# Optimization experiments

Hardware: AMD Instinct MI355X
Metric: run time of the kernel (lower is better)

The kernel has to match this reference:

```python
import jax, jax.numpy as jnp
import numpy as np

SOS = 0
MAX_LENGTH = 64

N_LATENTS = 256
N_CHARACTERS = 128
N_HIDDENS = 1024
BATCH = 4096


def setup_inputs() -> dict:
    key = jax.random.key(0)
    ks = jax.random.split(key, 16)
    H, L, C = N_HIDDENS, N_LATENTS, N_CHARACTERS
    s = 0.02
    return {
        "z": jax.random.normal(ks[0], (BATCH, L), dtype=jnp.float32),
        "embed_w": jax.random.normal(ks[1], (C, H), dtype=jnp.float32) * s,
        "z2h_w": jax.random.normal(ks[2], (H, L), dtype=jnp.float32) * s,
        "z2h_b": jnp.zeros((H,), dtype=jnp.float32),
        "w_ih0": jax.random.normal(ks[3], (3 * H, H + L), dtype=jnp.float32) * s,
        "w_hh0": jax.random.normal(ks[4], (3 * H, H), dtype=jnp.float32) * s,
        "b_ih0": jnp.zeros((3 * H,), dtype=jnp.float32),
        "b_hh0": jnp.zeros((3 * H,), dtype=jnp.float32),
        "w_ih1": jax.random.normal(ks[5], (3 * H, H), dtype=jnp.float32) * s,
        "w_hh1": jax.random.normal(ks[6], (3 * H, H), dtype=jnp.float32) * s,
        "b_ih1": jnp.zeros((3 * H,), dtype=jnp.float32),
        "b_hh1": jnp.zeros((3 * H,), dtype=jnp.float32),
        "h2o_w": jax.random.normal(ks[7], (C, H + L), dtype=jnp.float32) * s,
        "h2o_b": jnp.zeros((C,), dtype=jnp.float32),
    }


def _gru_cell(x, h, w_ih, w_hh, b_ih, b_hh):
    # PyTorch GRUCell math. x: [B, I], h: [B, H]
    gi = x @ w_ih.T + b_ih  # [B, 3H]
    gh = h @ w_hh.T + b_hh  # [B, 3H]
    i_r, i_z, i_n = jnp.split(gi, 3, axis=1)
    h_r, h_z, h_n = jnp.split(gh, 3, axis=1)
    r = jax.nn.sigmoid(i_r + h_r)
    zg = jax.nn.sigmoid(i_z + h_z)
    n = jnp.tanh(i_n + r * h_n)
    return (1.0 - zg) * n + zg * h


def reference(z, embed_w, z2h_w, z2h_b,
              w_ih0, w_hh0, b_ih0, b_hh0,
              w_ih1, w_hh1, b_ih1, b_hh1,
              h2o_w, h2o_b):
    batch = z.shape[0]
    h0 = z @ z2h_w.T + z2h_b  # [B, H], replicated across both GRU layers

    def step(carry, _):
        c_in, h1, h2 = carry
        e = embed_w[c_in]                      # [B, H] embedding lookup
        e = e * jax.nn.sigmoid(e)              # swish
        x = jnp.concatenate([e, z], axis=1)    # [B, H+L]
        h1 = _gru_cell(x, h1, w_ih0, w_hh0, b_ih0, b_hh0)
        h2 = _gru_cell(h1, h2, w_ih1, w_hh1, b_ih1, b_hh1)
        out = jnp.concatenate([h2, z], axis=1) @ h2o_w.T + h2o_b  # [B, C]
        # argmax(log_softmax(out)) == argmax(out)
        sample = jnp.argmax(out, axis=1).astype(jnp.int32)
        return (sample, h1, h2), out

    c0 = jnp.full((batch,), SOS, dtype=jnp.int32)
    _, outs = jax.lax.scan(step, (c0, h0, h0), None, length=MAX_LENGTH)
    return jnp.transpose(outs, (1, 0, 2))  # [B, T, C]
```

## Files before the change

### kernel.cpp

```cpp
#include <hip/hip_runtime.h>
#include <hip/hip_bf16.h>
#include <stdint.h>
#include <stddef.h>

#define B_   4096
#define H_   1024
#define L_   256
#define C_   128
#define T_   64
#define H3_  3072

typedef unsigned short u16;
typedef __attribute__((ext_vector_type(8))) short bf16x8;
typedef __attribute__((ext_vector_type(4))) float f32x4;

typedef const void __attribute__((address_space(1)))* as1_cvp;
typedef void __attribute__((address_space(3)))* as3_vp;

__device__ __forceinline__ void gl2lds16(const void* g, void* l) {
  __builtin_amdgcn_global_load_lds((as1_cvp)g, (as3_vp)l, 16, 0, 0);
}

__device__ __forceinline__ float bf2f(u16 u) {
  union { float f; unsigned int i; } x; x.i = ((unsigned int)u) << 16; return x.f;
}
__device__ __forceinline__ u16 f2bf(float f) {
  union { float f; unsigned int i; } x; x.f = f;
  unsigned int r = x.i + 0x7fffu + ((x.i >> 16) & 1u);
  return (u16)(r >> 16);
}
__device__ __forceinline__ float sigm(float x) { return 1.f / (1.f + __expf(-x)); }
__device__ __forceinline__ float tanh_fast(float x) {
  float e = __expf(2.f * x); return 1.f - 2.f / (e + 1.f);
}

template<int OUT_MODE>
__device__ __forceinline__ void gemm_tile_body(
    u16* As, u16* Ws,
    const u16* __restrict__ A, int lda,
    const u16* __restrict__ W, int ldw,
    const float* __restrict__ bias,
    void* __restrict__ C0p, void* __restrict__ C1p, int ldc, int K,
    int m0, int n0)
{
  const int tid  = threadIdx.x;
  const int wave = tid >> 6, lane = tid & 63;
  const int wm = (wave >> 1) * 64, wn = (wave & 1) * 64;
  const int lrow = lane & 15, lq = lane >> 4;
  const int arow = wave * 8 + (lane >> 3);
  const int acol = (lane & 7) * 8;

  f32x4 acc[4][4] = {};

  const u16* Ag = A + (size_t)m0 * lda;
  const u16* Wg = W + (size_t)n0 * ldw;

  for (int k0 = 0; k0 < K; k0 += 64) {
    __syncthreads();
    #pragma unroll
    for (int rd = 0; rd < 4; rd++) {
      gl2lds16(Ag + (size_t)(rd * 32 + arow) * lda + (k0 + acol), As + rd * 2048 + wave * 512);
      gl2lds16(Wg + (size_t)(rd * 32 + arow) * ldw + (k0 + acol), Ws + rd * 2048 + wave * 512);
    }
    __syncthreads();
    #pragma unroll
    for (int kk = 0; kk < 64; kk += 32) {
      bf16x8 af[4], bw[4];
      #pragma unroll
      for (int i = 0; i < 4; i++)
        af[i] = *(const bf16x8*)&As[(wm + i * 16 + lrow) * 64 + kk + lq * 8];
      #pragma unroll
      for (int j = 0; j < 4; j++)
        bw[j] = *(const bf16x8*)&Ws[(wn + j * 16 + lrow) * 64 + kk + lq * 8];
      #pragma unroll
      for (int i = 0; i < 4; i++)
        #pragma unroll
        for (int j = 0; j < 4; j++)
          acc[i][j] = __builtin_amdgcn_mfma_f32_16x16x32_bf16(af[i], bw[j], acc[i][j], 0, 0, 0);
    }
  }

  #pragma unroll
  for (int j = 0; j < 4; j++) {
    const int col = n0 + wn + j * 16 + lrow;
    const float bv = bias ? bias[col] : 0.f;
    #pragma unroll
    for (int i = 0; i < 4; i++) {
      #pragma unroll
      for (int r = 0; r < 4; r++) {
        const int row = m0 + wm + i * 16 + lq * 4 + r;
        float v = acc[i][j][r] + bv;
        if (OUT_MODE == 0) {
          ((float*)C0p)[(size_t)row * ldc + col] = v;
        } else if (OUT_MODE == 1) {
          ((u16*)C0p)[(size_t)row * ldc + col] = f2bf(v);
        } else {
          u16 hv = f2bf(v);
          ((u16*)C0p)[(size_t)row * ldc + col] = hv;
          ((u16*)C1p)[(size_t)row * ldc + col] = hv;
        }
      }
    }
  }
}

template<int OUT_MODE>
__global__ __launch_bounds__(256) void gemm_bt(
    const u16* __restrict__ A, int lda,
    const u16* __restrict__ W, int ldw,
    const float* __restrict__ bias,
    void* __restrict__ C0p, void* __restrict__ C1p, int ldc, int K)
{
  __shared__ __align__(16) u16 As[128 * 64];
  __shared__ __align__(16) u16 Ws[128 * 64];
  gemm_tile_body<OUT_MODE>(As, Ws, A, lda, W, ldw, bias, C0p, C1p, ldc, K,
                           blockIdx.y * 128, blockIdx.x * 128);
}

__device__ __forceinline__ void out_body(
    u16* As, u16* Ws, int ob,
    const u16* __restrict__ h2, const u16* __restrict__ Wo,
    const float* __restrict__ Oz, float* __restrict__ outp,
    int* __restrict__ cnew, int t)
{
  const int tid = threadIdx.x, wave = tid >> 6, lane = tid & 63;
  const int b0 = ob * 64;
  const int lrow = lane & 15, lq = lane >> 4;
  const int arow = wave * 8 + (lane >> 3);
  const int acol = (lane & 7) * 8;
  f32x4 acc[8] = {};

  for (int k0 = 0; k0 < H_; k0 += 64) {
    __syncthreads();
    #pragma unroll
    for (int rd = 0; rd < 2; rd++)
      gl2lds16(h2 + (size_t)(b0 + rd * 32 + arow) * H_ + k0 + acol, As + rd * 2048 + wave * 512);
    #pragma unroll
    for (int rd = 0; rd < 4; rd++)
      gl2lds16(Wo + (size_t)(rd * 32 + arow) * H_ + k0 + acol, Ws + rd * 2048 + wave * 512);
    __syncthreads();
    #pragma unroll
    for (int kk = 0; kk < 64; kk += 32) {
      bf16x8 af = *(const bf16x8*)&As[(wave * 16 + lrow) * 64 + kk + lq * 8];
      #pragma unroll
      for (int j = 0; j < 8; j++) {
        bf16x8 bw = *(const bf16x8*)&Ws[(j * 16 + lrow) * 64 + kk + lq * 8];
        acc[j] = __builtin_amdgcn_mfma_f32_16x16x32_bf16(af, bw, acc[j], 0, 0, 0);
      }
    }
  }

  #pragma unroll
  for (int r = 0; r < 4; r++) {
    const int row = b0 + wave * 16 + lq * 4 + r;
    float mv = -3.4e38f; int mi = 0;
    #pragma unroll
    for (int j = 0; j < 8; j++) {
      const int col = j * 16 + lrow;
      float v = acc[j][r] + Oz[(size_t)row * C_ + col];
      outp[(size_t)row * (T_ * C_) + t * C_ + col] = v;
      if (v > mv) { mv = v; mi = col; }
    }
    #pragma unroll
    for (int off = 1; off < 16; off <<= 1) {
      float ov = __shfl_xor(mv, off);
      int   oi = __shfl_xor(mi, off);
      if (ov > mv || (ov == mv && oi < mi)) { mv = ov; mi = oi; }
    }
    if (lrow == 0) cnew[row] = mi;
  }
}

__global__ __launch_bounds__(256) void step1(
    const u16* __restrict__ h1, const u16* __restrict__ whh0,
    const float* __restrict__ b_hh0, u16* __restrict__ gh0,
    const u16* __restrict__ h2cur, const u16* __restrict__ Wo,
    const float* __restrict__ Oz, float* __restrict__ outp,
    int* __restrict__ cbuf, int tprev)
{
  __shared__ __align__(16) u16 As[128 * 64];
  __shared__ __align__(16) u16 Ws[128 * 64];
  int bid = blockIdx.x;
  if (bid < 64) {
    if (tprev >= 0) out_body(As, Ws, bid, h2cur, Wo, Oz, outp, cbuf, tprev);
    return;
  }
  const int g = bid - 64;
  const int xcd = g & 7, k = g >> 3;
  const int n = xcd * 3 + (k % 3);
  const int m = k / 3;
  gemm_tile_body<1>(As, Ws, h1, H_, whh0, H_, b_hh0, gh0, nullptr, H3_, H_,
                    m * 128, n * 128);
}

template<bool PH2>
__device__ __forceinline__ void l3_phase(
    u16* As, u16* Ws,
    const u16* __restrict__ Ag, const u16* __restrict__ Wg, int j0,
    f32x4 acc[3][2][4], f32x4 accN[2][4])
{
  const int tid = threadIdx.x, wave = tid >> 6, lane = tid & 63;
  const int wmh = wave >> 1, wj = wave & 1;
  const int lrow = lane & 15, lq = lane >> 4;
  const int arow = wave * 8 + (lane >> 3);
  const int acol = (lane & 7) * 8;

  for (int k0 = 0; k0 < H_; k0 += 64) {
    __syncthreads();
    #pragma unroll
    for (int rd = 0; rd < 4; rd++)
      gl2lds16(Ag + (size_t)(rd * 32 + arow) * H_ + (k0 + acol), As + rd * 2048 + wave * 512);
    #pragma unroll
    for (int rd = 0; rd < 6; rd++)
      gl2lds16(Wg + (size_t)((rd >> 1) * 1024 + j0 + (rd & 1) * 32 + arow) * H_ + (k0 + acol),
               Ws + rd * 2048 + wave * 512);
    __syncthreads();
    #pragma unroll
    for (int kk = 0; kk < 64; kk += 32) {
      bf16x8 af[4];
      #pragma unroll
      for (int i = 0; i < 4; i++)
        af[i] = *(const bf16x8*)&As[(wmh * 64 + i * 16 + lrow) * 64 + kk + lq * 8];
      #pragma unroll
      for (int g = 0; g < 3; g++) {
        #pragma unroll
        for (int u = 0; u < 2; u++) {
          bf16x8 bw = *(const bf16x8*)&Ws[(g * 64 + wj * 32 + u * 16 + lrow) * 64 + kk + lq * 8];
          #pragma unroll
          for (int i = 0; i < 4; i++) {
            if (PH2 && g == 2)
              accN[u][i] = __builtin_amdgcn_mfma_f32_16x16x32_bf16(af[i], bw, accN[u][i], 0, 0, 0);
            else
              acc[g][u][i] = __builtin_amdgcn_mfma_f32_16x16x32_bf16(af[i], bw, acc[g][u][i], 0, 0, 0);
          }
        }
      }
    }
  }
}

__global__ __launch_bounds__(256, 2) void gemm_l3(
    const u16* __restrict__ h1, const u16* __restrict__ h2old,
    const u16* __restrict__ wih1, const u16* __restrict__ whh1,
    const float* __restrict__ b_ih1, const float* __restrict__ b_hh1,
    u16* __restrict__ h2new)
{
  __shared__ __align__(16) u16 As[128 * 64];
  __shared__ __align__(16) u16 Ws[192 * 64];
  const int bid = blockIdx.x;
  const int xcd = bid & 7, k = bid >> 3;
  const int jt = xcd * 2 + (k & 1);
  const int m  = k >> 1;
  const int m0 = m * 128, j0 = jt * 64;

  f32x4 acc[3][2][4] = {};
  f32x4 accN[2][4] = {};

  l3_phase<false>(As, Ws, h1    + (size_t)m0 * H_, wih1, j0, acc, accN);
  l3_phase<true >(As, Ws, h2old + (size_t)m0 * H_, whh1, j0, acc, accN);

  const int tid = threadIdx.x, wave = tid >> 6, lane = tid & 63;
  const int wmh = wave >> 1, wj = wave & 1;
  const int lrow = lane & 15, lq = lane >> 4;

  #pragma unroll
  for (int u = 0; u < 2; u++) {
    const int j = j0 + wj * 32 + u * 16 + lrow;
    const float bR  = b_ih1[j] + b_hh1[j];
    const float bZ  = b_ih1[H_ + j] + b_hh1[H_ + j];
    const float bNi = b_ih1[2 * H_ + j];
    const float bNh = b_hh1[2 * H_ + j];
    #pragma unroll
    for (int i = 0; i < 4; i++) {
      #pragma unroll
      for (int rr = 0; rr < 4; rr++) {
        const int row = m0 + wmh * 64 + i * 16 + lq * 4 + rr;
        float r  = sigm(acc[0][u][i][rr] + bR);
        float zg = sigm(acc[1][u][i][rr] + bZ);
        float nn = tanh_fast(acc[2][u][i][rr] + bNi + r * (accN[u][i][rr] + bNh));
        float hold = bf2f(h2old[(size_t)row * H_ + j]);
        h2new[(size_t)row * H_ + j] = f2bf((1.f - zg) * nn + zg * hold);
      }
    }
  }
}

__global__ __launch_bounds__(256) void gru_cell0_v(
    const int* __restrict__ c, const u16* __restrict__ Egi,
    const u16* __restrict__ Gz, const u16* __restrict__ gh,
    u16* __restrict__ h1)
{
  const int b = blockIdx.x, j = threadIdx.x * 4;
  const u16* eg = Egi + (size_t)c[b] * H3_ + j;
  const size_t g = (size_t)b * H3_ + j;
  ushort4 er = *(const ushort4*)&eg[0];
  ushort4 ez = *(const ushort4*)&eg[H_];
  ushort4 en = *(const ushort4*)&eg[2 * H_];
  ushort4 zr = *(const ushort4*)&Gz[g];
  ushort4 zz = *(const ushort4*)&Gz[g + H_];
  ushort4 zn = *(const ushort4*)&Gz[g + 2 * H_];
  ushort4 hr = *(const ushort4*)&gh[g];
  ushort4 hz = *(const ushort4*)&gh[g + H_];
  ushort4 hn = *(const ushort4*)&gh[g + 2 * H_];
  const size_t hi = (size_t)b * H_ + j;
  ushort4 hold = *(const ushort4*)&h1[hi];
  ushort4 outv;
  #pragma unroll
  for (int k = 0; k < 4; k++) {
    float gir = bf2f(((const u16*)&er)[k]) + bf2f(((const u16*)&zr)[k]);
    float giz = bf2f(((const u16*)&ez)[k]) + bf2f(((const u16*)&zz)[k]);
    float gin = bf2f(((const u16*)&en)[k]) + bf2f(((const u16*)&zn)[k]);
    float r  = sigm(gir + bf2f(((const u16*)&hr)[k]));
    float zg = sigm(giz + bf2f(((const u16*)&hz)[k]));
    float nn = tanh_fast(gin + r * bf2f(((const u16*)&hn)[k]));
    float h = bf2f(((const u16*)&hold)[k]);
    ((u16*)&outv)[k] = f2bf((1.f - zg) * nn + zg * h);
  }
  *(ushort4*)&h1[hi] = outv;
}

__global__ __launch_bounds__(256) void conv_bf16_k(const float* __restrict__ s, u16* __restrict__ d, int n) {
  int i = blockIdx.x * 256 + threadIdx.x;
  if (i < n) d[i] = f2bf(s[i]);
}
__global__ __launch_bounds__(256) void conv_split_k(const float* __restrict__ s, u16* __restrict__ dA,
                                                    u16* __restrict__ dZ, int rows) {
  int i = blockIdx.x * 256 + threadIdx.x;
  if (i >= rows * 1280) return;
  int rr = i / 1280, col = i - rr * 1280;
  float v = s[i];
  if (col < 1024) dA[(size_t)rr * 1024 + col] = f2bf(v);
  else            dZ[(size_t)rr * 256 + (col - 1024)] = f2bf(v);
}
__global__ __launch_bounds__(256) void conv_swish_k(const float* __restrict__ s, u16* __restrict__ d, int n) {
  int i = blockIdx.x * 256 + threadIdx.x;
  if (i < n) { float e = s[i]; d[i] = f2bf(e * sigm(e)); }
}

static inline char* wsal(char*& p, size_t bytes) {
  char* r = p; p += (bytes + 255) & ~(size_t)255; return r;
}

extern "C" void kernel_launch(void* const* d_in, const int* in_sizes, int n_in,
                              void* d_out, int out_size, void* d_ws, size_t ws_size,
                              hipStream_t stream) {
  const float* z       = (const float*)d_in[0];
  const float* embed_w = (const float*)d_in[1];
  const float* z2h_w   = (const float*)d_in[2];
  const float* z2h_b   = (const float*)d_in[3];
  const float* w_ih0   = (const float*)d_in[4];
  const float* w_hh0   = (const float*)d_in[5];
  const float* b_ih0   = (const float*)d_in[6];
  const float* b_hh0   = (const float*)d_in[7];
  const float* w_ih1   = (const float*)d_in[8];
  const float* w_hh1   = (const float*)d_in[9];
  const float* b_ih1   = (const float*)d_in[10];
  const float* b_hh1   = (const float*)d_in[11];
  const float* h2o_w   = (const float*)d_in[12];
  const float* h2o_b   = (const float*)d_in[13];
  float* outp = (float*)d_out;

  char* p = (char*)d_ws;
  u16* whh0  = (u16*)wsal(p, (size_t)H3_ * H_ * 2);
  u16* wih1  = (u16*)wsal(p, (size_t)H3_ * H_ * 2);
  u16* whh1  = (u16*)wsal(p, (size_t)H3_ * H_ * 2);
  u16* wih0a = (u16*)wsal(p, (size_t)H3_ * H_ * 2);
  u16* wih0z = (u16*)wsal(p, (size_t)H3_ * L_ * 2);
  u16* h2oa  = (u16*)wsal(p, (size_t)C_ * H_ * 2);
  u16* h2oz  = (u16*)wsal(p, (size_t)C_ * L_ * 2);
  u16* z2hb  = (u16*)wsal(p, (size_t)H_ * L_ * 2);
  u16* zb    = (u16*)wsal(p, (size_t)B_ * L_ * 2);
  u16* swe   = (u16*)wsal(p, (size_t)C_ * H_ * 2);
  u16* EgiB  = (u16*)wsal(p, (size_t)C_ * H3_ * 2);
  u16* Gz    = (u16*)wsal(p, (size_t)B_ * H3_ * 2);
  float* Oz  = (float*)wsal(p, (size_t)B_ * C_ * 4);
  u16* h1    = (u16*)wsal(p, (size_t)B_ * H_ * 2);
  u16* h2a   = (u16*)wsal(p, (size_t)B_ * H_ * 2);
  u16* h2b   = (u16*)wsal(p, (size_t)B_ * H_ * 2);
  u16* gh0   = (u16*)wsal(p, (size_t)B_ * H3_ * 2);
  int* cbuf  = (int*)wsal(p, (size_t)B_ * 4);

  conv_bf16_k<<<(B_*L_ + 255)/256, 256, 0, stream>>>(z, zb, B_*L_);
  conv_bf16_k<<<(H_*L_ + 255)/256, 256, 0, stream>>>(z2h_w, z2hb, H_*L_);
  conv_bf16_k<<<(H3_*H_ + 255)/256, 256, 0, stream>>>(w_hh0, whh0, H3_*H_);
  conv_bf16_k<<<(H3_*H_ + 255)/256, 256, 0, stream>>>(w_ih1, wih1, H3_*H_);
  conv_bf16_k<<<(H3_*H_ + 255)/256, 256, 0, stream>>>(w_hh1, whh1, H3_*H_);
  conv_split_k<<<(H3_*1280 + 255)/256, 256, 0, stream>>>(w_ih0, wih0a, wih0z, H3_);
  conv_split_k<<<(C_*1280 + 255)/256, 256, 0, stream>>>(h2o_w, h2oa, h2oz, C_);
  conv_swish_k<<<(C_*H_ + 255)/256, 256, 0, stream>>>(embed_w, swe, C_*H_);
  hipMemsetAsync(cbuf, 0, B_ * sizeof(int), stream);

  gemm_bt<2><<<dim3(H_/128, B_/128), 256, 0, stream>>>(zb, L_, z2hb, L_, z2h_b, h1, h2a, H_, L_);
  gemm_bt<1><<<dim3(H3_/128, 1), 256, 0, stream>>>(swe, H_, wih0a, H_, b_ih0, EgiB, nullptr, H3_, H_);
  gemm_bt<1><<<dim3(H3_/128, B_/128), 256, 0, stream>>>(zb, L_, wih0z, L_, nullptr, Gz, nullptr, H3_, L_);
  gemm_bt<0><<<dim3(1, B_/128), 256, 0, stream>>>(zb, L_, h2oz, L_, h2o_b, Oz, nullptr, C_, L_);

  for (int t = 0; t < T_; t++) {
    const u16* h2cur = (t & 1) ? h2b : h2a;
    u16*       h2nxt = (t & 1) ? h2a : h2b;
    step1<<<832, 256, 0, stream>>>(h1, whh0, b_hh0, gh0, h2cur, h2oa, Oz, outp, cbuf, t - 1);
    gru_cell0_v<<<B_, 256, 0, stream>>>(cbuf, EgiB, Gz, gh0, h1);
    gemm_l3<<<512, 256, 0, stream>>>(h1, h2cur, wih1, whh1, b_ih1, b_hh1, h2nxt);
  }
  step1<<<64, 256, 0, stream>>>(h1, whh0, b_hh0, gh0, h2a, h2oa, Oz, outp, cbuf, T_ - 1);
}
```

Measured before the change: 8.406 ms.

## Fuse layer-0 hidden GEMM with GRU gate epilogue and split output projection

The layer-0 hidden GEMM now uses the GRU gate tiling and applies the full gate math in its epilogue. That removes the separate elementwise GRU kernel and the write and re-read of the 3H-wide gh0 buffer on every step. h1 is now double-buffered, so the new state does not overwrite the old state the epilogue still reads. The output projection and argmax move into a standalone 64-block kernel after layer 1, so it no longer overlaps with the hidden GEMM. The fused epilogue also makes narrow per-element gathers from Egi and Gz.

```diff
diff --git a/kernel.cpp b/kernel.cpp
--- a/kernel.cpp
+++ b/kernel.cpp
@@ -117,82 +117,6 @@
                            blockIdx.y * 128, blockIdx.x * 128);
 }
 
-__device__ __forceinline__ void out_body(
-    u16* As, u16* Ws, int ob,
-    const u16* __restrict__ h2, const u16* __restrict__ Wo,
-    const float* __restrict__ Oz, float* __restrict__ outp,
-    int* __restrict__ cnew, int t)
-{
-  const int tid = threadIdx.x, wave = tid >> 6, lane = tid & 63;
-  const int b0 = ob * 64;
-  const int lrow = lane & 15, lq = lane >> 4;
-  const int arow = wave * 8 + (lane >> 3);
-  const int acol = (lane & 7) * 8;
-  f32x4 acc[8] = {};
-
-  for (int k0 = 0; k0 < H_; k0 += 64) {
-    __syncthreads();
-    #pragma unroll
-    for (int rd = 0; rd < 2; rd++)
-      gl2lds16(h2 + (size_t)(b0 + rd * 32 + arow) * H_ + k0 + acol, As + rd * 2048 + wave * 512);
-    #pragma unroll
-    for (int rd = 0; rd < 4; rd++)
-      gl2lds16(Wo + (size_t)(rd * 32 + arow) * H_ + k0 + acol, Ws + rd * 2048 + wave * 512);
-    __syncthreads();
-    #pragma unroll
-    for (int kk = 0; kk < 64; kk += 32) {
-      bf16x8 af = *(const bf16x8*)&As[(wave * 16 + lrow) * 64 + kk + lq * 8];
-      #pragma unroll
-      for (int j = 0; j < 8; j++) {
-        bf16x8 bw = *(const bf16x8*)&Ws[(j * 16 + lrow) * 64 + kk + lq * 8];
-        acc[j] = __builtin_amdgcn_mfma_f32_16x16x32_bf16(af, bw, acc[j], 0, 0, 0);
-      }
-    }
-  }
-
-  #pragma unroll
-  for (int r = 0; r < 4; r++) {
-    const int row = b0 + wave * 16 + lq * 4 + r;
-    float mv = -3.4e38f; int mi = 0;
-    #pragma unroll
-    for (int j = 0; j < 8; j++) {
-      const int col = j * 16 + lrow;
-      float v = acc[j][r] + Oz[(size_t)row * C_ + col];
-      outp[(size_t)row * (T_ * C_) + t * C_ + col] = v;
-      if (v > mv) { mv = v; mi = col; }
-    }
-    #pragma unroll
-    for (int off = 1; off < 16; off <<= 1) {
-      float ov = __shfl_xor(mv, off);
-      int   oi = __shfl_xor(mi, off);
-      if (ov > mv || (ov == mv && oi < mi)) { mv = ov; mi = oi; }
-    }
-    if (lrow == 0) cnew[row] = mi;
-  }
-}
-
-__global__ __launch_bounds__(256) void step1(
-    const u16* __restrict__ h1, const u16* __restrict__ whh0,
-    const float* __restrict__ b_hh0, u16* __restrict__ gh0,
-    const u16* __restrict__ h2cur, const u16* __restrict__ Wo,
-    const float* __restrict__ Oz, float* __restrict__ outp,
-    int* __restrict__ cbuf, int tprev)
-{
-  __shared__ __align__(16) u16 As[128 * 64];
-  __shared__ __align__(16) u16 Ws[128 * 64];
-  int bid = blockIdx.x;
-  if (bid < 64) {
-    if (tprev >= 0) out_body(As, Ws, bid, h2cur, Wo, Oz, outp, cbuf, tprev);
-    return;
-  }
-  const int g = bid - 64;
-  const int xcd = g & 7, k = g >> 3;
-  const int n = xcd * 3 + (k % 3);
-  const int m = k / 3;
-  gemm_tile_body<1>(As, Ws, h1, H_, whh0, H_, b_hh0, gh0, nullptr, H3_, H_,
-                    m * 128, n * 128);
-}
-
 template<bool PH2>
 __device__ __forceinline__ void l3_phase(
     u16* As, u16* Ws,
@@ -239,6 +163,56 @@
   }
 }
 
+__global__ __launch_bounds__(256, 2) void gates0_fused(
+    const u16* __restrict__ h1old, const u16* __restrict__ whh0,
+    const float* __restrict__ b_hh0,
+    const int* __restrict__ c, const u16* __restrict__ Egi,
+    const u16* __restrict__ Gz, u16* __restrict__ h1new)
+{
+  __shared__ __align__(16) u16 As[128 * 64];
+  __shared__ __align__(16) u16 Ws[192 * 64];
+  const int bid = blockIdx.x;
+  const int xcd = bid & 7, k = bid >> 3;
+  const int jt = xcd * 2 + (k & 1);
+  const int m  = k >> 1;
+  const int m0 = m * 128, j0 = jt * 64;
+
+  f32x4 acc[3][2][4] = {};
+  f32x4 accN[2][4];
+
+  l3_phase<false>(As, Ws, h1old + (size_t)m0 * H_, whh0, j0, acc, accN);
+
+  const int tid = threadIdx.x, wave = tid >> 6, lane = tid & 63;
+  const int wmh = wave >> 1, wj = wave & 1;
+  const int lrow = lane & 15, lq = lane >> 4;
+
+  #pragma unroll
+  for (int i = 0; i < 4; i++) {
+    #pragma unroll
+    for (int rr = 0; rr < 4; rr++) {
+      const int row = m0 + wmh * 64 + i * 16 + lq * 4 + rr;
+      const int cv = c[row];
+      const u16* eg = Egi + (size_t)cv * H3_;
+      const u16* gz = Gz + (size_t)row * H3_;
+      #pragma unroll
+      for (int u = 0; u < 2; u++) {
+        const int j = j0 + wj * 32 + u * 16 + lrow;
+        float gir = bf2f(eg[j])          + bf2f(gz[j]);
+        float giz = bf2f(eg[H_ + j])     + bf2f(gz[H_ + j]);
+        float gin = bf2f(eg[2 * H_ + j]) + bf2f(gz[2 * H_ + j]);
+        float ghr = acc[0][u][i][rr] + b_hh0[j];
+        float ghz = acc[1][u][i][rr] + b_hh0[H_ + j];
+        float ghn = acc[2][u][i][rr] + b_hh0[2 * H_ + j];
+        float r  = sigm(gir + ghr);
+        float zg = sigm(giz + ghz);
+        float nn = tanh_fast(gin + r * ghn);
+        float hold = bf2f(h1old[(size_t)row * H_ + j]);
+        h1new[(size_t)row * H_ + j] = f2bf((1.f - zg) * nn + zg * hold);
+      }
+    }
+  }
+}
+
 __global__ __launch_bounds__(256, 2) void gemm_l3(
     const u16* __restrict__ h1, const u16* __restrict__ h2old,
     const u16* __restrict__ wih1, const u16* __restrict__ whh1,
@@ -285,38 +259,59 @@
   }
 }
 
-__global__ __launch_bounds__(256) void gru_cell0_v(
-    const int* __restrict__ c, const u16* __restrict__ Egi,
-    const u16* __restrict__ Gz, const u16* __restrict__ gh,
-    u16* __restrict__ h1)
-{
-  const int b = blockIdx.x, j = threadIdx.x * 4;
-  const u16* eg = Egi + (size_t)c[b] * H3_ + j;
-  const size_t g = (size_t)b * H3_ + j;
-  ushort4 er = *(const ushort4*)&eg[0];
-  ushort4 ez = *(const ushort4*)&eg[H_];
-  ushort4 en = *(const ushort4*)&eg[2 * H_];
-  ushort4 zr = *(const ushort4*)&Gz[g];
-  ushort4 zz = *(const ushort4*)&Gz[g + H_];
-  ushort4 zn = *(const ushort4*)&Gz[g + 2 * H_];
-  ushort4 hr = *(const ushort4*)&gh[g];
-  ushort4 hz = *(const ushort4*)&gh[g + H_];
-  ushort4 hn = *(const ushort4*)&gh[g + 2 * H_];
-  const size_t hi = (size_t)b * H_ + j;
-  ushort4 hold = *(const ushort4*)&h1[hi];
-  ushort4 outv;
+__global__ __launch_bounds__(256) void out_only(
+    const u16* __restrict__ h2, const u16* __restrict__ Wo,
+    const float* __restrict__ Oz, float* __restrict__ outp,
+    int* __restrict__ cnew, int t)
+{
+  __shared__ __align__(16) u16 As[64 * 64];
+  __shared__ __align__(16) u16 Ws[128 * 64];
+  const int tid = threadIdx.x, wave = tid >> 6, lane = tid & 63;
+  const int b0 = blockIdx.x * 64;
+  const int lrow = lane & 15, lq = lane >> 4;
+  const int arow = wave * 8 + (lane >> 3);
+  const int acol = (lane & 7) * 8;
+  f32x4 acc[8] = {};
+
+  for (int k0 = 0; k0 < H_; k0 += 64) {
+    __syncthreads();
+    #pragma unroll
+    for (int rd = 0; rd < 2; rd++)
+      gl2lds16(h2 + (size_t)(b0 + rd * 32 + arow) * H_ + k0 + acol, As + rd * 2048 + wave * 512);
+    #pragma unroll
+    for (int rd = 0; rd < 4; rd++)
+      gl2lds16(Wo + (size_t)(rd * 32 + arow) * H_ + k0 + acol, Ws + rd * 2048 + wave * 512);
+    __syncthreads();
+    #pragma unroll
+    for (int kk = 0; kk < 64; kk += 32) {
+      bf16x8 af = *(const bf16x8*)&As[(wave * 16 + lrow) * 64 + kk + lq * 8];
+      #pragma unroll
+      for (int j = 0; j < 8; j++) {
+        bf16x8 bw = *(const bf16x8*)&Ws[(j * 16 + lrow) * 64 + kk + lq * 8];
+        acc[j] = __builtin_amdgcn_mfma_f32_16x16x32_bf16(af, bw, acc[j], 0, 0, 0);
+      }
+    }
+  }
+
   #pragma unroll
-  for (int k = 0; k < 4; k++) {
-    float gir = bf2f(((const u16*)&er)[k]) + bf2f(((const u16*)&zr)[k]);
-    float giz = bf2f(((const u16*)&ez)[k]) + bf2f(((const u16*)&zz)[k]);
-    float gin = bf2f(((const u16*)&en)[k]) + bf2f(((const u16*)&zn)[k]);
-    float r  = sigm(gir + bf2f(((const u16*)&hr)[k]));
-    float zg = sigm(giz + bf2f(((const u16*)&hz)[k]));
-    float nn = tanh_fast(gin + r * bf2f(((const u16*)&hn)[k]));
-    float h = bf2f(((const u16*)&hold)[k]);
-    ((u16*)&outv)[k] = f2bf((1.f - zg) * nn + zg * h);
-  }
-  *(ushort4*)&h1[hi] = outv;
+  for (int r = 0; r < 4; r++) {
+    const int row = b0 + wave * 16 + lq * 4 + r;
+    float mv = -3.4e38f; int mi = 0;
+    #pragma unroll
+    for (int j = 0; j < 8; j++) {
+      const int col = j * 16 + lrow;
+      float v = acc[j][r] + Oz[(size_t)row * C_ + col];
+      outp[(size_t)row * (T_ * C_) + t * C_ + col] = v;
+      if (v > mv) { mv = v; mi = col; }
+    }
+    #pragma unroll
+    for (int off = 1; off < 16; off <<= 1) {
+      float ov = __shfl_xor(mv, off);
+      int   oi = __shfl_xor(mi, off);
+      if (ov > mv || (ov == mv && oi < mi)) { mv = ov; mi = oi; }
+    }
+    if (lrow == 0) cnew[row] = mi;
+  }
 }
 
 __global__ __launch_bounds__(256) void conv_bf16_k(const float* __restrict__ s, u16* __restrict__ d, int n) {
@@ -374,10 +369,10 @@
   u16* EgiB  = (u16*)wsal(p, (size_t)C_ * H3_ * 2);
   u16* Gz    = (u16*)wsal(p, (size_t)B_ * H3_ * 2);
   float* Oz  = (float*)wsal(p, (size_t)B_ * C_ * 4);
-  u16* h1    = (u16*)wsal(p, (size_t)B_ * H_ * 2);
+  u16* h1a   = (u16*)wsal(p, (size_t)B_ * H_ * 2);
+  u16* h1b   = (u16*)wsal(p, (size_t)B_ * H_ * 2);
   u16* h2a   = (u16*)wsal(p, (size_t)B_ * H_ * 2);
   u16* h2b   = (u16*)wsal(p, (size_t)B_ * H_ * 2);
-  u16* gh0   = (u16*)wsal(p, (size_t)B_ * H3_ * 2);
   int* cbuf  = (int*)wsal(p, (size_t)B_ * 4);
 
   conv_bf16_k<<<(B_*L_ + 255)/256, 256, 0, stream>>>(z, zb, B_*L_);
@@ -390,17 +385,18 @@
   conv_swish_k<<<(C_*H_ + 255)/256, 256, 0, stream>>>(embed_w, swe, C_*H_);
   hipMemsetAsync(cbuf, 0, B_ * sizeof(int), stream);
 
-  gemm_bt<2><<<dim3(H_/128, B_/128), 256, 0, stream>>>(zb, L_, z2hb, L_, z2h_b, h1, h2a, H_, L_);
+  gemm_bt<2><<<dim3(H_/128, B_/128), 256, 0, stream>>>(zb, L_, z2hb, L_, z2h_b, h1a, h2a, H_, L_);
   gemm_bt<1><<<dim3(H3_/128, 1), 256, 0, stream>>>(swe, H_, wih0a, H_, b_ih0, EgiB, nullptr, H3_, H_);
   gemm_bt<1><<<dim3(H3_/128, B_/128), 256, 0, stream>>>(zb, L_, wih0z, L_, nullptr, Gz, nullptr, H3_, L_);
   gemm_bt<0><<<dim3(1, B_/128), 256, 0, stream>>>(zb, L_, h2oz, L_, h2o_b, Oz, nullptr, C_, L_);
 
+  u16 *h1c = h1a, *h1n = h1b, *h2c = h2a, *h2n = h2b;
   for (int t = 0; t < T_; t++) {
-    const u16* h2cur = (t & 1) ? h2b : h2a;
-    u16*       h2nxt = (t & 1) ? h2a : h2b;
-    step1<<<832, 256, 0, stream>>>(h1, whh0, b_hh0, gh0, h2cur, h2oa, Oz, outp, cbuf, t - 1);
-    gru_cell0_v<<<B_, 256, 0, stream>>>(cbuf, EgiB, Gz, gh0, h1);
-    gemm_l3<<<512, 256, 0, stream>>>(h1, h2cur, wih1, whh1, b_ih1, b_hh1, h2nxt);
-  }
-  step1<<<64, 256, 0, stream>>>(h1, whh0, b_hh0, gh0, h2a, h2oa, Oz, outp, cbuf, T_ - 1);
-}
+    gates0_fused<<<512, 256, 0, stream>>>(h1c, whh0, b_hh0, cbuf, EgiB, Gz, h1n);
+    gemm_l3<<<512, 256, 0, stream>>>(h1n, h2c, wih1, whh1, b_ih1, b_hh1, h2n);
+    out_only<<<64, 256, 0, stream>>>(h2n, h2oa, Oz, outp, cbuf, t);
+    u16* tmp;
+    tmp = h1c; h1c = h1n; h1n = tmp;
+    tmp = h2c; h2c = h2n; h2n = tmp;
+  }
+}
```

Result: slower. 10.25 ms (+21.9%).
